# Kernel optimization log

Measured on AMD Instinct MI355X. Metric: run time of the kernel, lower is better.

Reference implementation:

```python
import jax, jax.numpy as jnp
import numpy as np

N, F, H, T = 100000, 128, 128, 10
E = 1600000
NUM_GRAPHS = 512
BN_EPS = 1e-5


def setup_inputs() -> dict:
    key = jax.random.key(0)
    ks = jax.random.split(key, 16)
    x = jax.random.normal(ks[0], (N, F), dtype=jnp.float32)
    edge_index = jax.random.randint(ks[1], (2, E), 0, N, dtype=jnp.int64)
    batch = jnp.sort(jax.random.randint(ks[2], (N,), 0, NUM_GRAPHS, dtype=jnp.int64))
    s = lambda fin: 1.0 / np.sqrt(fin)
    return {
        "x": x, "edge_index": edge_index, "batch": batch,
        # GINConv 1 MLP: Linear(F,H) -> BN(H) -> ReLU -> Linear(H,H)
        "W1a": jax.random.uniform(ks[3], (F, H), jnp.float32, -s(F), s(F)),
        "b1a": jax.random.uniform(ks[4], (H,), jnp.float32, -s(F), s(F)),
        "g1": jnp.ones((H,), jnp.float32),
        "bt1": jnp.zeros((H,), jnp.float32),
        "W1b": jax.random.uniform(ks[5], (H, H), jnp.float32, -s(H), s(H)),
        "b1b": jax.random.uniform(ks[6], (H,), jnp.float32, -s(H), s(H)),
        # GINConv 2 MLP
        "W2a": jax.random.uniform(ks[7], (H, H), jnp.float32, -s(H), s(H)),
        "b2a": jax.random.uniform(ks[8], (H,), jnp.float32, -s(H), s(H)),
        "g2": jnp.ones((H,), jnp.float32),
        "bt2": jnp.zeros((H,), jnp.float32),
        "W2b": jax.random.uniform(ks[9], (H, H), jnp.float32, -s(H), s(H)),
        "b2b": jax.random.uniform(ks[10], (H,), jnp.float32, -s(H), s(H)),
        # final Linear(H, T)
        "Wl": jax.random.uniform(ks[11], (H, T), jnp.float32, -s(H), s(H)),
        "bl": jax.random.uniform(ks[12], (T,), jnp.float32, -s(H), s(H)),
    }


def _batchnorm(h, gamma, beta):
    # training-mode BN over the node dimension (biased variance), eps=1e-5
    mean = jnp.mean(h, axis=0)
    var = jnp.mean(jnp.square(h - mean), axis=0)
    return (h - mean) * jax.lax.rsqrt(var + BN_EPS) * gamma + beta


def _gin_conv(x, edge_index, Wa, ba, gamma, beta, Wb, bb):
    src, dst = edge_index[0], edge_index[1]
    # sum-aggregate neighbor messages: scatter-add x[src] into dst rows
    agg = jax.ops.segment_sum(x[src], dst, num_segments=x.shape[0])
    h = (x + agg) @ Wa + ba          # eps=0 in GINConv default
    h = jax.nn.relu(_batchnorm(h, gamma, beta))
    return h @ Wb + bb


def reference(x, edge_index, batch, W1a, b1a, g1, bt1, W1b, b1b,
              W2a, b2a, g2, bt2, W2b, b2b, Wl, bl):
    h = jax.nn.relu(_gin_conv(x, edge_index, W1a, b1a, g1, bt1, W1b, b1b))
    h = jax.nn.relu(_gin_conv(h, edge_index, W2a, b2a, g2, bt2, W2b, b2b))
    pooled = jax.ops.segment_sum(h, batch, num_segments=NUM_GRAPHS)  # [G, H]
    return pooled @ Wl + bl  # [G, T]
```

## Files before the change

kernel.cpp:

```cpp
#include <hip/hip_runtime.h>
#include <cstdint>
#include <cstddef>

#define NFEAT 128
#define TGRAPH 10
#define NGRAPHS 512
#define BN_EPS 1e-5f
#define BIN_CHUNK 2048
#define GSPAN 8
#define TSTR 24
#define ATSTR 40

typedef __attribute__((ext_vector_type(8))) short bf16x8;
typedef __attribute__((ext_vector_type(4))) float f32x4;
typedef __attribute__((ext_vector_type(2))) float f32x2;

__device__ __forceinline__ float bf2f(short s) {
    union { unsigned u; float f; } c;
    c.u = ((unsigned)(unsigned short)s) << 16;
    return c.f;
}
__device__ __forceinline__ short f2bf(float f) {
    union { float f; unsigned u; } c;
    c.f = f;
    unsigned u = c.u;
    return (short)((u + 0x7fffu + ((u >> 16) & 1u)) >> 16);
}
__device__ __forceinline__ void accp(f32x2& a, unsigned v) {
    union { unsigned u; float f; } lo, hi;
    lo.u = v << 16;
    hi.u = v & 0xffff0000u;
    f32x2 t;
    t[0] = lo.f;
    t[1] = hi.f;
    a += t;
}


__global__ void k_bucket_scan(const int* __restrict__ bhist, int* __restrict__ bbase,
                              int* __restrict__ cur256, int E) {
    __shared__ int s[256];
    int t = threadIdx.x;
    int v = bhist[t];
    s[t] = v;
    __syncthreads();
    for (int off = 1; off < 256; off <<= 1) {
        int x = 0;
        if (t >= off) x = s[t - off];
        __syncthreads();
        if (t >= off) s[t] += x;
        __syncthreads();
    }
    int excl = s[t] - v;
    bbase[t] = excl;
    cur256[t] = excl;
    if (t == 255) bbase[256] = E;
}

__global__ __launch_bounds__(256) void k_bin_scatter(const int* __restrict__ src,
                                                     const int* __restrict__ dst,
                                                     int* __restrict__ cur256,
                                                     int2* __restrict__ binned, int E) {
    __shared__ int hist[256];
    __shared__ int base[256];
    int t = threadIdx.x;
    int e0 = blockIdx.x * BIN_CHUNK;
    int e1 = min(e0 + BIN_CHUNK, E);
    hist[t] = 0;
    __syncthreads();
    for (int e = e0 + t; e < e1; e += 256) {
        int b = dst[e] >> 9;
        atomicAdd(&hist[b], 1);
    }
    __syncthreads();
    int c = hist[t];
    if (c > 0) base[t] = atomicAdd(&cur256[t], c);
    __syncthreads();
    hist[t] = 0;
    __syncthreads();
    for (int e = e0 + t; e < e1; e += 256) {
        int d = dst[e];
        int b = d >> 9;
        int loc = atomicAdd(&hist[b], 1);
        binned[base[b] + loc] = make_int2(src[e], d);
    }
}

__global__ __launch_bounds__(512) void k_bucket_csr(const int2* __restrict__ binned,
                                                    const int* __restrict__ bbase,
                                                    int* __restrict__ rowptr,
                                                    int* __restrict__ adj,
                                                    int N, int E, int nb) {
    __shared__ int deg[512];
    __shared__ int cur[512];
    int b = blockIdx.x;
    int t = threadIdx.x;
    int e0 = bbase[b], e1 = bbase[b + 1];
    deg[t] = 0;
    __syncthreads();
    for (int e = e0 + t; e < e1; e += 512)
        atomicAdd(&deg[binned[e].y & 511], 1);
    __syncthreads();
    int v = deg[t];
    for (int off = 1; off < 512; off <<= 1) {
        int x = 0;
        if (t >= off) x = deg[t - off];
        __syncthreads();
        if (t >= off) deg[t] += x;
        __syncthreads();
    }
    int excl = deg[t] - v;
    cur[t] = excl;
    int node = b * 512 + t;
    if (node < N) rowptr[node] = e0 + excl;
    if (b == nb - 1 && t == 0) rowptr[N] = E;
    __syncthreads();
    for (int e = e0 + t; e < e1; e += 512) {
        int2 p = binned[e];
        int loc = atomicAdd(&cur[p.y & 511], 1);
        adj[e0 + loc] = p.x;
    }
}

__global__ __launch_bounds__(256) void k_prep_hist(const int* __restrict__ dst,
                                                   int* __restrict__ bhist, int E, int hb,
                                                   const float* __restrict__ x,
                                                   short* __restrict__ xbf,
                                                   const float* __restrict__ W0,
                                                   const float* __restrict__ W1,
                                                   const float* __restrict__ W2,
                                                   const float* __restrict__ W3,
                                                   short* __restrict__ Wf, int n4) {
    int t = threadIdx.x;
    if (blockIdx.x < hb) {
        __shared__ int h[256];
        h[t] = 0;
        __syncthreads();
        for (int e = blockIdx.x * 256 + t; e < E; e += hb * 256)
            atomicAdd(&h[dst[e] >> 9], 1);
        __syncthreads();
        if (h[t]) atomicAdd(&bhist[t], h[t]);
        return;
    }
    int i = (blockIdx.x - hb) * 256 + t;
    if (i < n4) {
        float4 v = ((const float4*)x)[i];
        ushort4 o;
        o.x = (unsigned short)f2bf(v.x);
        o.y = (unsigned short)f2bf(v.y);
        o.z = (unsigned short)f2bf(v.z);
        o.w = (unsigned short)f2bf(v.w);
        ((ushort4*)xbf)[i] = o;
    } else {
        int idx = i - n4;
        if (idx < 4 * 16384) {
            int w = idx >> 14, r = idx & 16383;
            int j = r & 7, lane = (r >> 3) & 63, ct = (r >> 9) & 7, kc = r >> 12;
            int k = kc * 32 + (lane >> 4) * 8 + j;
            int n = ct * 16 + (lane & 15);
            const float* W = (w == 0) ? W0 : (w == 1) ? W1 : (w == 2) ? W2 : W3;
            Wf[idx] = f2bf(W[k * NFEAT + n]);
        }
    }
}

__global__ __launch_bounds__(256) void k_agg_gemm(const short* __restrict__ X,
                                                  const int* __restrict__ rowptr,
                                                  const int* __restrict__ adj,
                                                  const short* __restrict__ Wf,
                                                  const float* __restrict__ bias,
                                                  float* __restrict__ stats,
                                                  short* __restrict__ C, int N) {
    __shared__ float s_aux[256];
    __shared__ short c_tile[4][16 * ATSTR];
    int tid = threadIdx.x;
    int wave = tid >> 6, lane = tid & 63;
    int quad = lane >> 4, l16 = lane & 15;
    int row_base = blockIdx.x * 64 + wave * 16;

    s_aux[tid] = 0.f;
    __syncthreads();

    const uint4* Xv = (const uint4*)X;

    f32x2 acc[4][4];
#pragma unroll
    for (int kc = 0; kc < 4; ++kc)
#pragma unroll
        for (int m = 0; m < 4; ++m) acc[kc][m] = (f32x2){0.f, 0.f};

    int r = row_base + l16;
    if (r < N) {
        size_t rb = (size_t)r * 16 + quad;
#pragma unroll
        for (int kc = 0; kc < 4; ++kc) {
            uint4 v = Xv[rb + kc * 4];
            accp(acc[kc][0], v.x); accp(acc[kc][1], v.y);
            accp(acc[kc][2], v.z); accp(acc[kc][3], v.w);
        }
        int e0 = rowptr[r], e1 = rowptr[r + 1];
        int a0 = (e0 < e1) ? adj[e0] : 0;
        int a1 = (e0 + 1 < e1) ? adj[e0 + 1] : -1;
        for (int e = e0; e < e1; e += 2) {
            int p0 = a0;
            int p1 = a1;
            a0 = (e + 2 < e1) ? adj[e + 2] : 0;
            a1 = (e + 3 < e1) ? adj[e + 3] : -1;
            size_t n0 = (size_t)p0 * 16 + quad;
            uint4 u0[4], u1[4];
#pragma unroll
            for (int kc = 0; kc < 4; ++kc) u0[kc] = Xv[n0 + kc * 4];
            if (p1 >= 0) {
                size_t n1 = (size_t)p1 * 16 + quad;
#pragma unroll
                for (int kc = 0; kc < 4; ++kc) u1[kc] = Xv[n1 + kc * 4];
            } else {
#pragma unroll
                for (int kc = 0; kc < 4; ++kc) u1[kc] = make_uint4(0u, 0u, 0u, 0u);
            }
#pragma unroll
            for (int kc = 0; kc < 4; ++kc) {
                accp(acc[kc][0], u0[kc].x); accp(acc[kc][1], u0[kc].y);
                accp(acc[kc][2], u0[kc].z); accp(acc[kc][3], u0[kc].w);
                accp(acc[kc][0], u1[kc].x); accp(acc[kc][1], u1[kc].y);
                accp(acc[kc][2], u1[kc].z); accp(acc[kc][3], u1[kc].w);
            }
        }
    }

    bf16x8 afrag[4];
#pragma unroll
    for (int kc = 0; kc < 4; ++kc) {
        bf16x8 f;
#pragma unroll
        for (int m = 0; m < 4; ++m) {
            f[2 * m] = f2bf(acc[kc][m][0]);
            f[2 * m + 1] = f2bf(acc[kc][m][1]);
        }
        afrag[kc] = f;
    }

    f32x4 oacc[8];
#pragma unroll
    for (int j = 0; j < 8; j++) oacc[j] = (f32x4){0.f, 0.f, 0.f, 0.f};

#pragma unroll
    for (int kc = 0; kc < 4; ++kc) {
        const short* wp = Wf + ((size_t)(kc * 8) * 64 + lane) * 8;
#pragma unroll
        for (int ct = 0; ct < 8; ++ct) {
            bf16x8 b = *(const bf16x8*)(wp + (size_t)ct * 64 * 8);
            oacc[ct] = __builtin_amdgcn_mfma_f32_16x16x32_bf16(afrag[kc], b, oacc[ct], 0, 0, 0);
        }
    }

    short* tile = &c_tile[wave][0];
    int row2 = lane >> 2, q2 = lane & 3;
#pragma unroll
    for (int ct = 0; ct < 8; ++ct) {
        int col = ct * 16 + l16;
        float bv = bias[col];
        float ls = 0.f, ls2 = 0.f;
#pragma unroll
        for (int reg = 0; reg < 4; ++reg) {
            int lrow = quad * 4 + reg;
            float v = oacc[ct][reg] + bv;
            if (row_base + lrow < N) { ls += v; ls2 += v * v; }
            tile[lrow * ATSTR + (ct & 1) * 16 + l16] = f2bf(v);
        }
        ls += __shfl_xor(ls, 16);
        ls += __shfl_xor(ls, 32);
        ls2 += __shfl_xor(ls2, 16);
        ls2 += __shfl_xor(ls2, 32);
        if (quad == 0) {
            atomicAdd(&s_aux[col], ls);
            atomicAdd(&s_aux[NFEAT + col], ls2);
        }
        if (ct & 1) {
            uint4 val = *(const uint4*)(tile + row2 * ATSTR + q2 * 8);
            int grow = row_base + row2;
            if (grow < N) {
                int col0 = (ct - 1) * 16 + q2 * 8;
                size_t addr = ((size_t)(grow >> 4) * 4 + (col0 >> 5)) * 512 +
                              (size_t)((((col0 >> 3) & 3) * 16 + (grow & 15)) * 8);
                *(uint4*)(C + addr) = val;
            }
        }
    }

    __syncthreads();
    if (tid < NFEAT) {
        atomicAdd(&stats[tid], s_aux[tid]);
        atomicAdd(&stats[NFEAT + tid], s_aux[NFEAT + tid]);
    }
}

template <bool BN_RELU_IN, bool RELU_OUT, bool STATS, bool FRAG_OUT, bool POOL>
__global__ __launch_bounds__(256) void k_gemm_mfma(const short* __restrict__ A,
                                                   const short* __restrict__ Wf,
                                                   const float* __restrict__ bias,
                                                   float* __restrict__ stats,
                                                   const float* __restrict__ gamma,
                                                   const float* __restrict__ beta,
                                                   const int* __restrict__ batch,
                                                   float* __restrict__ pooled,
                                                   short* __restrict__ C, int N) {
    __shared__ float s_aux[256];
    __shared__ short c_tile[4][32 * TSTR];
    __shared__ float s_pool[GSPAN][NFEAT];
    int tid = threadIdx.x;
    int wave = tid >> 6, lane = tid & 63;
    int quad = lane >> 4, l16 = lane & 15;
    int row_base = blockIdx.x * 128 + wave * 32;

    int gbase = 0;
    if constexpr (POOL) {
        int first = blockIdx.x * 128;
        gbase = (first < N) ? batch[first] : 0;
        for (int i = tid; i < GSPAN * NFEAT; i += 256) s_pool[i >> 7][i & 127] = 0.f;
    }
    if constexpr (STATS) s_aux[tid] = 0.f;
    if constexpr (BN_RELU_IN) {
        if (tid < NFEAT) {
            float mean = stats[tid] / (float)N;
            float var = stats[NFEAT + tid] / (float)N - mean * mean;
            float inv = rsqrtf(var + BN_EPS);
            float sc = gamma[tid] * inv;
            s_aux[tid] = sc;
            s_aux[NFEAT + tid] = beta[tid] - mean * sc;
        }
    }
    if constexpr (STATS || BN_RELU_IN || POOL) __syncthreads();

    f32x4 acc[2][8];
#pragma unroll
    for (int i = 0; i < 2; i++)
#pragma unroll
        for (int j = 0; j < 8; j++) acc[i][j] = (f32x4){0.f, 0.f, 0.f, 0.f};

    const short* af = A + ((size_t)(blockIdx.x * 8 + wave * 2) * 4) * 512;

#pragma unroll
    for (int kc = 0; kc < 4; ++kc) {
        bf16x8 a0 = *(const bf16x8*)(af + (size_t)kc * 512 + lane * 8);
        bf16x8 a1 = *(const bf16x8*)(af + (size_t)(4 + kc) * 512 + lane * 8);
        if constexpr (BN_RELU_IN) {
            int koff = kc * 32 + quad * 8;
#pragma unroll
            for (int j = 0; j < 8; j++) {
                float sc = s_aux[koff + j];
                float sh = s_aux[NFEAT + koff + j];
                a0[j] = f2bf(fmaxf(bf2f(a0[j]) * sc + sh, 0.f));
                a1[j] = f2bf(fmaxf(bf2f(a1[j]) * sc + sh, 0.f));
            }
        }
        const short* wp = Wf + ((size_t)(kc * 8) * 64 + lane) * 8;
#pragma unroll
        for (int ct = 0; ct < 8; ++ct) {
            bf16x8 b = *(const bf16x8*)(wp + (size_t)ct * 64 * 8);
            acc[0][ct] = __builtin_amdgcn_mfma_f32_16x16x32_bf16(a0, b, acc[0][ct], 0, 0, 0);
            acc[1][ct] = __builtin_amdgcn_mfma_f32_16x16x32_bf16(a1, b, acc[1][ct], 0, 0, 0);
        }
    }

    int dg[8];
    if constexpr (POOL) {
#pragma unroll
        for (int rt = 0; rt < 2; ++rt)
#pragma unroll
            for (int reg = 0; reg < 4; ++reg) {
                int row = row_base + rt * 16 + quad * 4 + reg;
                dg[rt * 4 + reg] = (row < N) ? (batch[row] - gbase) : -1;
            }
    }

    short* tile = &c_tile[wave][0];
    int row2 = lane >> 1, half = lane & 1;
#pragma unroll
    for (int ct = 0; ct < 8; ++ct) {
        int col = ct * 16 + l16;
        float bv = bias[col];
        float ls = 0.f, ls2 = 0.f;
        int cg = -1;
        float ps = 0.f;
#pragma unroll
        for (int rt = 0; rt < 2; ++rt) {
#pragma unroll
            for (int reg = 0; reg < 4; ++reg) {
                int lrow = rt * 16 + quad * 4 + reg;
                float v = acc[rt][ct][reg] + bv;
                if constexpr (RELU_OUT) v = fmaxf(v, 0.f);
                if constexpr (STATS) {
                    if (row_base + lrow < N) { ls += v; ls2 += v * v; }
                }
                if constexpr (POOL) {
                    int d = dg[rt * 4 + reg];
                    if (d != cg) {
                        if (cg >= 0) atomicAdd(&s_pool[cg & (GSPAN - 1)][col], ps);
                        cg = d; ps = 0.f;
                    }
                    if (d >= 0) ps += v;
                } else {
                    tile[lrow * TSTR + l16] = f2bf(v);
                }
            }
        }
        if constexpr (POOL) {
            if (cg >= 0) atomicAdd(&s_pool[cg & (GSPAN - 1)][col], ps);
        }
        if constexpr (STATS) {
            ls += __shfl_xor(ls, 16);
            ls += __shfl_xor(ls, 32);
            ls2 += __shfl_xor(ls2, 16);
            ls2 += __shfl_xor(ls2, 32);
            if (quad == 0) {
                atomicAdd(&s_aux[col], ls);
                atomicAdd(&s_aux[NFEAT + col], ls2);
            }
        }
        if constexpr (!POOL) {
            uint4 val = *(const uint4*)(tile + row2 * TSTR + half * 8);
            int grow = row_base + row2;
            if (grow < N) {
                int col0 = ct * 16 + half * 8;
                if constexpr (FRAG_OUT) {
                    size_t addr = ((size_t)(grow >> 4) * 4 + (col0 >> 5)) * 512 +
                                  (size_t)((((col0 >> 3) & 3) * 16 + (grow & 15)) * 8);
                    *(uint4*)(C + addr) = val;
                } else {
                    *(uint4*)(C + (size_t)grow * NFEAT + col0) = val;
                }
            }
        }
    }

    if constexpr (STATS) {
        __syncthreads();
        if (tid < NFEAT) {
            atomicAdd(&stats[tid], s_aux[tid]);
            atomicAdd(&stats[NFEAT + tid], s_aux[NFEAT + tid]);
        }
    }
    if constexpr (POOL) {
        __syncthreads();
        for (int i = tid; i < GSPAN * NFEAT; i += 256) {
            float v = s_pool[i >> 7][i & 127];
            if (v != 0.f) {
                int gg = gbase + (i >> 7);
                if (gg < NGRAPHS) atomicAdd(&pooled[gg * NFEAT + (i & 127)], v);
            }
        }
    }
}

__global__ void k_final(const float* __restrict__ pooled, const float* __restrict__ Wl,
                        const float* __restrict__ bl, float* __restrict__ out) {
    int idx = blockIdx.x * blockDim.x + threadIdx.x;
    if (idx >= NGRAPHS * TGRAPH) return;
    int g = idx / TGRAPH, t = idx % TGRAPH;
    const float* p = pooled + (size_t)g * NFEAT;
    float acc = bl[t];
#pragma unroll 16
    for (int k = 0; k < NFEAT; ++k) acc += p[k] * Wl[k * TGRAPH + t];
    out[idx] = acc;
}

extern "C" void kernel_launch(void* const* d_in, const int* in_sizes, int n_in,
                              void* d_out, int out_size, void* d_ws, size_t ws_size,
                              hipStream_t stream) {
    const float* x = (const float*)d_in[0];
    const int* ei = (const int*)d_in[1];
    const int* batch = (const int*)d_in[2];
    const float* W1a = (const float*)d_in[3];
    const float* b1a = (const float*)d_in[4];
    const float* g1 = (const float*)d_in[5];
    const float* bt1 = (const float*)d_in[6];
    const float* W1b = (const float*)d_in[7];
    const float* b1b = (const float*)d_in[8];
    const float* W2a = (const float*)d_in[9];
    const float* b2a = (const float*)d_in[10];
    const float* g2 = (const float*)d_in[11];
    const float* bt2 = (const float*)d_in[12];
    const float* W2b = (const float*)d_in[13];
    const float* b2b = (const float*)d_in[14];
    const float* Wl = (const float*)d_in[15];
    const float* bl = (const float*)d_in[16];
    float* out = (float*)d_out;

    int N = in_sizes[2];
    int E = in_sizes[1] / 2;
    int nb = (N + 511) >> 9;
    const int* src = ei;
    const int* dst = ei + E;

    int gemmBlocks = (N + 127) / 128;
    int padRows = gemmBlocks * 128;
    int aggBlocks = (N + 63) / 64;

    char* ws = (char*)d_ws;
    size_t off = 0;
    auto alloc = [&](size_t bytes) -> void* {
        void* p = ws + off;
        off = (off + bytes + 255) & ~(size_t)255;
        return p;
    };
    short* xbf = (short*)alloc((size_t)N * NFEAT * 2);
    short* ybf = (short*)alloc((size_t)padRows * NFEAT * 2);
    short* hbf = (short*)alloc((size_t)N * NFEAT * 2);
    short* Wf = (short*)alloc((size_t)4 * 16384 * 2);
    int* adj = (int*)alloc((size_t)E * 4);
    int2* binned = (int2*)alloc((size_t)E * 8);
    int* rowptr = (int*)alloc((size_t)(N + 1) * 4);
    int* bbase = (int*)alloc(257 * 4);
    int* cur256 = (int*)alloc(256 * 4);
    int* bhist = (int*)alloc(256 * 4);
    float* stats1 = (float*)alloc(256 * 4);
    float* stats2 = (float*)alloc(256 * 4);
    float* pooled = (float*)alloc((size_t)NGRAPHS * NFEAT * 4);
    size_t zbytes = (char*)(pooled + (size_t)NGRAPHS * NFEAT) - (char*)bhist;

    hipMemsetAsync(bhist, 0, zbytes, stream);

    int n4 = N * NFEAT / 4;
    int prepTot = n4 + 4 * 16384;
    int hb = 784;
    k_prep_hist<<<hb + (prepTot + 255) / 256, 256, 0, stream>>>(
        dst, bhist, E, hb, x, xbf, W1a, W1b, W2a, W2b, Wf, n4);
    k_bucket_scan<<<1, 256, 0, stream>>>(bhist, bbase, cur256, E);
    k_bin_scatter<<<(E + BIN_CHUNK - 1) / BIN_CHUNK, 256, 0, stream>>>(src, dst, cur256, binned, E);
    k_bucket_csr<<<nb, 512, 0, stream>>>(binned, bbase, rowptr, adj, N, E, nb);

    k_agg_gemm<<<aggBlocks, 256, 0, stream>>>(xbf, rowptr, adj, Wf + 0 * 16384, b1a,
                                              stats1, ybf, N);
    k_gemm_mfma<true, true, false, false, false><<<gemmBlocks, 256, 0, stream>>>(
        ybf, Wf + 1 * 16384, b1b, stats1, g1, bt1, nullptr, nullptr, hbf, N);

    k_agg_gemm<<<aggBlocks, 256, 0, stream>>>(hbf, rowptr, adj, Wf + 2 * 16384, b2a,
                                              stats2, ybf, N);
    k_gemm_mfma<true, true, false, false, true><<<gemmBlocks, 256, 0, stream>>>(
        ybf, Wf + 3 * 16384, b2b, stats2, g2, bt2, batch, pooled, nullptr, N);

    k_final<<<(NGRAPHS * TGRAPH + 255) / 256, 256, 0, stream>>>(pooled, Wl, bl, out);
}
```

Measured before the change: 445.3 us.

## Sort nodes by degree within buckets to balance aggregation waves

The CSR build kernel now emits a per-512-node-bucket permutation that orders nodes by descending in-degree, padding empty slots with -1. The aggregation+GEMM kernel processes 16-row tiles of permuted nodes so that lanes within a wave have similar neighbor counts, which cuts divergence in the gather loop. Blocks shrink to 128 threads, and downstream GEMM/pool kernels read rows through the permutation, scattering outputs back to original row order. This adds an extra scan in the CSR kernel, indirect row indices, and less coalesced writes and batch lookups.

```diff
diff --git a/kernel.cpp b/kernel.cpp
--- a/kernel.cpp
+++ b/kernel.cpp
@@ -90,6 +90,7 @@
                                                     const int* __restrict__ bbase,
                                                     int* __restrict__ rowptr,
                                                     int* __restrict__ adj,
+                                                    int* __restrict__ perm,
                                                     int N, int E, int nb) {
     __shared__ int deg[512];
     __shared__ int cur[512];
@@ -119,6 +120,30 @@
         int2 p = binned[e];
         int loc = atomicAdd(&cur[p.y & 511], 1);
         adj[e0 + loc] = p.x;
+    }
+    __syncthreads();
+    int dcl = min(v, 255);
+    if (t < 256) deg[t] = 0;
+    __syncthreads();
+    if (node < N) atomicAdd(&deg[dcl], 1);
+    __syncthreads();
+    if (t < 256) cur[t] = deg[255 - t];
+    __syncthreads();
+    for (int off = 1; off < 256; off <<= 1) {
+        int x = 0;
+        if (t >= off && t < 256) x = cur[t - off];
+        __syncthreads();
+        if (t >= off && t < 256) cur[t] += x;
+        __syncthreads();
+    }
+    if (t < 256) {
+        int d = 255 - t;
+        deg[d] = cur[t] - deg[d];
+    }
+    __syncthreads();
+    if (node < N) {
+        int p = atomicAdd(&deg[dcl], 1);
+        perm[b * 512 + p] = node;
     }
 }
 
@@ -164,22 +189,28 @@
     }
 }
 
-__global__ __launch_bounds__(256) void k_agg_gemm(const short* __restrict__ X,
+__global__ __launch_bounds__(128) void k_agg_gemm(const short* __restrict__ X,
                                                   const int* __restrict__ rowptr,
                                                   const int* __restrict__ adj,
+                                                  const int* __restrict__ perm,
                                                   const short* __restrict__ Wf,
                                                   const float* __restrict__ bias,
                                                   float* __restrict__ stats,
                                                   short* __restrict__ C, int N) {
     __shared__ float s_aux[256];
-    __shared__ short c_tile[4][16 * ATSTR];
+    __shared__ short c_tile[2][16 * ATSTR];
+    __shared__ int s_rows[2][16];
     int tid = threadIdx.x;
     int wave = tid >> 6, lane = tid & 63;
     int quad = lane >> 4, l16 = lane & 15;
-    int row_base = blockIdx.x * 64 + wave * 16;
+    int tile = blockIdx.x * 2 + wave;
 
     s_aux[tid] = 0.f;
-    __syncthreads();
+    s_aux[tid + 128] = 0.f;
+    __syncthreads();
+
+    int r = perm[tile * 16 + l16];
+    if (quad == 0) s_rows[wave][l16] = r;
 
     const uint4* Xv = (const uint4*)X;
 
@@ -189,8 +220,7 @@
 #pragma unroll
         for (int m = 0; m < 4; ++m) acc[kc][m] = (f32x2){0.f, 0.f};
 
-    int r = row_base + l16;
-    if (r < N) {
+    if (r >= 0) {
         size_t rb = (size_t)r * 16 + quad;
 #pragma unroll
         for (int kc = 0; kc < 4; ++kc) {
@@ -254,7 +284,7 @@
         }
     }
 
-    short* tile = &c_tile[wave][0];
+    short* tilep = &c_tile[wave][0];
     int row2 = lane >> 2, q2 = lane & 3;
 #pragma unroll
     for (int ct = 0; ct < 8; ++ct) {
@@ -265,8 +295,8 @@
         for (int reg = 0; reg < 4; ++reg) {
             int lrow = quad * 4 + reg;
             float v = oacc[ct][reg] + bv;
-            if (row_base + lrow < N) { ls += v; ls2 += v * v; }
-            tile[lrow * ATSTR + (ct & 1) * 16 + l16] = f2bf(v);
+            if (s_rows[wave][lrow] >= 0) { ls += v; ls2 += v * v; }
+            tilep[lrow * ATSTR + (ct & 1) * 16 + l16] = f2bf(v);
         }
         ls += __shfl_xor(ls, 16);
         ls += __shfl_xor(ls, 32);
@@ -277,60 +307,58 @@
             atomicAdd(&s_aux[NFEAT + col], ls2);
         }
         if (ct & 1) {
-            uint4 val = *(const uint4*)(tile + row2 * ATSTR + q2 * 8);
-            int grow = row_base + row2;
-            if (grow < N) {
-                int col0 = (ct - 1) * 16 + q2 * 8;
-                size_t addr = ((size_t)(grow >> 4) * 4 + (col0 >> 5)) * 512 +
-                              (size_t)((((col0 >> 3) & 3) * 16 + (grow & 15)) * 8);
-                *(uint4*)(C + addr) = val;
-            }
-        }
-    }
-
-    __syncthreads();
-    if (tid < NFEAT) {
-        atomicAdd(&stats[tid], s_aux[tid]);
-        atomicAdd(&stats[NFEAT + tid], s_aux[NFEAT + tid]);
-    }
-}
-
-template <bool BN_RELU_IN, bool RELU_OUT, bool STATS, bool FRAG_OUT, bool POOL>
-__global__ __launch_bounds__(256) void k_gemm_mfma(const short* __restrict__ A,
-                                                   const short* __restrict__ Wf,
-                                                   const float* __restrict__ bias,
-                                                   float* __restrict__ stats,
-                                                   const float* __restrict__ gamma,
-                                                   const float* __restrict__ beta,
-                                                   const int* __restrict__ batch,
-                                                   float* __restrict__ pooled,
-                                                   short* __restrict__ C, int N) {
+            uint4 val = *(const uint4*)(tilep + row2 * ATSTR + q2 * 8);
+            int col0 = (ct - 1) * 16 + q2 * 8;
+            size_t addr = ((size_t)tile * 4 + (col0 >> 5)) * 512 +
+                          (size_t)((((col0 >> 3) & 3) * 16 + row2) * 8);
+            *(uint4*)(C + addr) = val;
+        }
+    }
+
+    __syncthreads();
+    for (int i = tid; i < NFEAT; i += 128) {
+        atomicAdd(&stats[i], s_aux[i]);
+        atomicAdd(&stats[NFEAT + i], s_aux[NFEAT + i]);
+    }
+}
+
+template <bool POOL>
+__global__ __launch_bounds__(256) void k_gemm_bn(const short* __restrict__ A,
+                                                 const short* __restrict__ Wf,
+                                                 const float* __restrict__ bias,
+                                                 const float* __restrict__ stats,
+                                                 const float* __restrict__ gamma,
+                                                 const float* __restrict__ beta,
+                                                 const int* __restrict__ perm,
+                                                 const int* __restrict__ batch,
+                                                 float* __restrict__ pooled,
+                                                 short* __restrict__ C, int N) {
     __shared__ float s_aux[256];
     __shared__ short c_tile[4][32 * TSTR];
     __shared__ float s_pool[GSPAN][NFEAT];
+    __shared__ int s_rows[4][32];
     int tid = threadIdx.x;
     int wave = tid >> 6, lane = tid & 63;
     int quad = lane >> 4, l16 = lane & 15;
-    int row_base = blockIdx.x * 128 + wave * 32;
+    int posbase = blockIdx.x * 128 + wave * 32;
+
+    if (lane < 32) s_rows[wave][lane] = perm[posbase + lane];
 
     int gbase = 0;
     if constexpr (POOL) {
-        int first = blockIdx.x * 128;
-        gbase = (first < N) ? batch[first] : 0;
+        int cb = (blockIdx.x * 128) & ~511;
+        gbase = batch[min(cb, N - 1)];
         for (int i = tid; i < GSPAN * NFEAT; i += 256) s_pool[i >> 7][i & 127] = 0.f;
     }
-    if constexpr (STATS) s_aux[tid] = 0.f;
-    if constexpr (BN_RELU_IN) {
-        if (tid < NFEAT) {
-            float mean = stats[tid] / (float)N;
-            float var = stats[NFEAT + tid] / (float)N - mean * mean;
-            float inv = rsqrtf(var + BN_EPS);
-            float sc = gamma[tid] * inv;
-            s_aux[tid] = sc;
-            s_aux[NFEAT + tid] = beta[tid] - mean * sc;
-        }
-    }
-    if constexpr (STATS || BN_RELU_IN || POOL) __syncthreads();
+    if (tid < NFEAT) {
+        float mean = stats[tid] / (float)N;
+        float var = stats[NFEAT + tid] / (float)N - mean * mean;
+        float inv = rsqrtf(var + BN_EPS);
+        float sc = gamma[tid] * inv;
+        s_aux[tid] = sc;
+        s_aux[NFEAT + tid] = beta[tid] - mean * sc;
+    }
+    __syncthreads();
 
     f32x4 acc[2][8];
 #pragma unroll
@@ -344,15 +372,13 @@
     for (int kc = 0; kc < 4; ++kc) {
         bf16x8 a0 = *(const bf16x8*)(af + (size_t)kc * 512 + lane * 8);
         bf16x8 a1 = *(const bf16x8*)(af + (size_t)(4 + kc) * 512 + lane * 8);
-        if constexpr (BN_RELU_IN) {
-            int koff = kc * 32 + quad * 8;
-#pragma unroll
-            for (int j = 0; j < 8; j++) {
-                float sc = s_aux[koff + j];
-                float sh = s_aux[NFEAT + koff + j];
-                a0[j] = f2bf(fmaxf(bf2f(a0[j]) * sc + sh, 0.f));
-                a1[j] = f2bf(fmaxf(bf2f(a1[j]) * sc + sh, 0.f));
-            }
+        int koff = kc * 32 + quad * 8;
+#pragma unroll
+        for (int j = 0; j < 8; j++) {
+            float sc = s_aux[koff + j];
+            float sh = s_aux[NFEAT + koff + j];
+            a0[j] = f2bf(fmaxf(bf2f(a0[j]) * sc + sh, 0.f));
+            a1[j] = f2bf(fmaxf(bf2f(a1[j]) * sc + sh, 0.f));
         }
         const short* wp = Wf + ((size_t)(kc * 8) * 64 + lane) * 8;
 #pragma unroll
@@ -369,8 +395,8 @@
         for (int rt = 0; rt < 2; ++rt)
 #pragma unroll
             for (int reg = 0; reg < 4; ++reg) {
-                int row = row_base + rt * 16 + quad * 4 + reg;
-                dg[rt * 4 + reg] = (row < N) ? (batch[row] - gbase) : -1;
+                int rr = s_rows[wave][rt * 16 + quad * 4 + reg];
+                dg[rt * 4 + reg] = (rr >= 0) ? (batch[rr] - gbase) : -1;
             }
     }
 
@@ -380,7 +406,6 @@
     for (int ct = 0; ct < 8; ++ct) {
         int col = ct * 16 + l16;
         float bv = bias[col];
-        float ls = 0.f, ls2 = 0.f;
         int cg = -1;
         float ps = 0.f;
 #pragma unroll
@@ -388,11 +413,7 @@
 #pragma unroll
             for (int reg = 0; reg < 4; ++reg) {
                 int lrow = rt * 16 + quad * 4 + reg;
-                float v = acc[rt][ct][reg] + bv;
-                if constexpr (RELU_OUT) v = fmaxf(v, 0.f);
-                if constexpr (STATS) {
-                    if (row_base + lrow < N) { ls += v; ls2 += v * v; }
-                }
+                float v = fmaxf(acc[rt][ct][reg] + bv, 0.f);
                 if constexpr (POOL) {
                     int d = dg[rt * 4 + reg];
                     if (d != cg) {
@@ -407,40 +428,16 @@
         }
         if constexpr (POOL) {
             if (cg >= 0) atomicAdd(&s_pool[cg & (GSPAN - 1)][col], ps);
-        }
-        if constexpr (STATS) {
-            ls += __shfl_xor(ls, 16);
-            ls += __shfl_xor(ls, 32);
-            ls2 += __shfl_xor(ls2, 16);
-            ls2 += __shfl_xor(ls2, 32);
-            if (quad == 0) {
-                atomicAdd(&s_aux[col], ls);
-                atomicAdd(&s_aux[NFEAT + col], ls2);
+        } else {
+            uint4 val = *(const uint4*)(tile + row2 * TSTR + half * 8);
+            int grow = s_rows[wave][row2];
+            if (grow >= 0) {
+                int col0 = ct * 16 + half * 8;
+                *(uint4*)(C + (size_t)grow * NFEAT + col0) = val;
             }
         }
-        if constexpr (!POOL) {
-            uint4 val = *(const uint4*)(tile + row2 * TSTR + half * 8);
-            int grow = row_base + row2;
-            if (grow < N) {
-                int col0 = ct * 16 + half * 8;
-                if constexpr (FRAG_OUT) {
-                    size_t addr = ((size_t)(grow >> 4) * 4 + (col0 >> 5)) * 512 +
-                                  (size_t)((((col0 >> 3) & 3) * 16 + (grow & 15)) * 8);
-                    *(uint4*)(C + addr) = val;
-                } else {
-                    *(uint4*)(C + (size_t)grow * NFEAT + col0) = val;
-                }
-            }
-        }
-    }
-
-    if constexpr (STATS) {
-        __syncthreads();
-        if (tid < NFEAT) {
-            atomicAdd(&stats[tid], s_aux[tid]);
-            atomicAdd(&stats[NFEAT + tid], s_aux[NFEAT + tid]);
-        }
-    }
+    }
+
     if constexpr (POOL) {
         __syncthreads();
         for (int i = tid; i < GSPAN * NFEAT; i += 256) {
@@ -495,7 +492,7 @@
 
     int gemmBlocks = (N + 127) / 128;
     int padRows = gemmBlocks * 128;
-    int aggBlocks = (N + 63) / 64;
+    int aggBlocks = gemmBlocks * 4;
 
     char* ws = (char*)d_ws;
     size_t off = 0;
@@ -511,6 +508,7 @@
     int* adj = (int*)alloc((size_t)E * 4);
     int2* binned = (int2*)alloc((size_t)E * 8);
     int* rowptr = (int*)alloc((size_t)(N + 1) * 4);
+    int* perm = (int*)alloc((size_t)nb * 512 * 4);
     int* bbase = (int*)alloc(257 * 4);
     int* cur256 = (int*)alloc(256 * 4);
     int* bhist = (int*)alloc(256 * 4);
@@ -520,6 +518,7 @@
     size_t zbytes = (char*)(pooled + (size_t)NGRAPHS * NFEAT) - (char*)bhist;
 
     hipMemsetAsync(bhist, 0, zbytes, stream);
+    hipMemsetAsync(perm, 0xFF, (size_t)nb * 512 * 4, stream);
 
     int n4 = N * NFEAT / 4;
     int prepTot = n4 + 4 * 16384;
@@ -528,17 +527,17 @@
         dst, bhist, E, hb, x, xbf, W1a, W1b, W2a, W2b, Wf, n4);
     k_bucket_scan<<<1, 256, 0, stream>>>(bhist, bbase, cur256, E);
     k_bin_scatter<<<(E + BIN_CHUNK - 1) / BIN_CHUNK, 256, 0, stream>>>(src, dst, cur256, binned, E);
-    k_bucket_csr<<<nb, 512, 0, stream>>>(binned, bbase, rowptr, adj, N, E, nb);
-
-    k_agg_gemm<<<aggBlocks, 256, 0, stream>>>(xbf, rowptr, adj, Wf + 0 * 16384, b1a,
+    k_bucket_csr<<<nb, 512, 0, stream>>>(binned, bbase, rowptr, adj, perm, N, E, nb);
+
+    k_agg_gemm<<<aggBlocks, 128, 0, stream>>>(xbf, rowptr, adj, perm, Wf + 0 * 16384, b1a,
                                               stats1, ybf, N);
-    k_gemm_mfma<true, true, false, false, false><<<gemmBlocks, 256, 0, stream>>>(
-        ybf, Wf + 1 * 16384, b1b, stats1, g1, bt1, nullptr, nullptr, hbf, N);
-
-    k_agg_gemm<<<aggBlocks, 256, 0, stream>>>(hbf, rowptr, adj, Wf + 2 * 16384, b2a,
+    k_gemm_bn<false><<<gemmBlocks, 256, 0, stream>>>(
+        ybf, Wf + 1 * 16384, b1b, stats1, g1, bt1, perm, nullptr, nullptr, hbf, N);
+
+    k_agg_gemm<<<aggBlocks, 128, 0, stream>>>(hbf, rowptr, adj, perm, Wf + 2 * 16384, b2a,
                                               stats2, ybf, N);
-    k_gemm_mfma<true, true, false, false, true><<<gemmBlocks, 256, 0, stream>>>(
-        ybf, Wf + 3 * 16384, b2b, stats2, g2, bt2, batch, pooled, nullptr, N);
+    k_gemm_bn<true><<<gemmBlocks, 256, 0, stream>>>(
+        ybf, Wf + 3 * 16384, b2b, stats2, g2, bt2, perm, batch, pooled, nullptr, N);
 
     k_final<<<(NGRAPHS * TGRAPH + 255) / 256, 256, 0, stream>>>(pooled, Wl, bl, out);
 }
```

Result: slower. 496.9 us (+11.6%).
